# Kernel tuning notes

Measured on AMD Instinct MI355X. Metric: run time of the kernel, lower is better.

Reference implementation:

```python
import jax, jax.numpy as jnp
from jax import lax
import numpy as np

# TopoLoss(dim=1, p=2, topo_lambda=1.0)
# p=2 -> Euclidean ground metric for the Vietoris-Rips filtration.
# This reference computes the dominant H0 persistence diagram of the VR complex:
# for a point cloud, H0 births are all 0 and deaths are exactly the MST edge
# weights (Kruskal/union-find == Prim, computed here with a fixed-length scan).
# Wasserstein distance between the two diagrams (equal cardinality N-1, births 0)
# reduces to optimal 1D matching of the sorted death values (q=1, the
# torch_topological WassersteinDistance default).
TOPO_LAMBDA = 1.0
EPS = 1e-12


def _pairwise_euclidean(x):
    # x: [B, N, D] -> [B, N, N] via the Gram trick (avoids [B,N,N,D] temp)
    sq = jnp.sum(x * x, axis=-1)                      # [B, N]
    g = jnp.einsum('bnd,bmd->bnm', x, x)              # [B, N, N]
    d2 = sq[:, :, None] + sq[:, None, :] - 2.0 * g
    return jnp.sqrt(jnp.maximum(d2, 0.0) + EPS)


def _mst_deaths(D):
    # Prim's algorithm on a dense distance matrix D: [N, N].
    # Returns the sorted MST edge weights = H0 death times ([N-1]).
    N = D.shape[0]
    inf = jnp.asarray(jnp.inf, D.dtype)
    in_tree0 = jnp.zeros((N,), bool).at[0].set(True)
    min_dist0 = D[0]

    def step(carry, _):
        in_tree, min_dist = carry
        masked = jnp.where(in_tree, inf, min_dist)
        j = jnp.argmin(masked)
        death = masked[j]
        in_tree = in_tree.at[j].set(True)
        min_dist = jnp.minimum(min_dist, D[j])
        return (in_tree, min_dist), death

    _, deaths = lax.scan(step, (in_tree0, min_dist0), None, length=N - 1)
    return jnp.sort(deaths)


def _h0_diagram_deaths(x):
    # x: [B, N, D] -> sorted death values [B, N-1]
    D = _pairwise_euclidean(x)
    return jax.vmap(_mst_deaths)(D)


def setup_inputs() -> dict:
    key = jax.random.key(0)
    k1, k2 = jax.random.split(key)
    B, N, D = 64, 1024, 3
    gts = jax.random.normal(k1, (B, N, D), dtype=jnp.float32)
    preds = jax.random.normal(k2, (B, N, D), dtype=jnp.float32)
    return {"gts": gts, "preds": preds}


def reference(gts, preds):
    # note: source names pers_info_pred = complex(gts) (vars swapped there);
    # Wasserstein is symmetric so ordering is irrelevant.
    deaths_a = _h0_diagram_deaths(gts)    # [B, N-1]
    deaths_b = _h0_diagram_deaths(preds)  # [B, N-1]
    # W1 between diagrams with equal cardinality and births==0:
    # optimal matching of sorted death coordinates.
    per_batch = jnp.sum(jnp.abs(deaths_a - deaths_b), axis=-1)  # [B]
    return per_batch.mean() * TOPO_LAMBDA
```

## Files before the change

### kernel.cpp

```cpp
#include <hip/hip_runtime.h>
#include <math.h>

#define N 1024
#define T 1024
#define HALF 512
#define PHASE_CAP 10
#define SWITCH 80

typedef float v2f __attribute__((ext_vector_type(2)));
typedef unsigned long long ull;

#define INF64 0xFFFFFFFFFFFFFFFFull
#define INF32 0xFFFFFFFFu

__device__ __forceinline__ unsigned umin32(unsigned a, unsigned b) { return a < b ? a : b; }
__device__ __forceinline__ unsigned umax32(unsigned a, unsigned b) { return a > b ? a : b; }
__device__ __forceinline__ int imin32(int a, int b) { return a < b ? a : b; }

__device__ __forceinline__ unsigned walk_root(const unsigned* parent, unsigned x) {
    unsigned prev = x, cur = parent[x];
    while (cur != prev) {
        unsigned nxt = parent[cur];
        if (nxt == prev) { cur = umin32(cur, prev); break; }
        prev = cur; cur = nxt;
    }
    return cur;
}

#define DPP_MIN_SHR(v, sh)                                                                   \
    do {                                                                                     \
        unsigned _t = (unsigned)__builtin_amdgcn_update_dpp(                                 \
            (int)0xFFFFFFFF, (int)(v), 0x110 | (sh), 0xF, 0xF, false);                       \
        (v) = umin32((v), _t);                                                               \
    } while (0)

__global__ __launch_bounds__(T) void scan1_kernel(const float* __restrict__ gts,
                                                  const float* __restrict__ preds,
                                                  unsigned* __restrict__ bests1) {
    __shared__ float px[N], py[N], pz[N];
    __shared__ float stage[3 * N];
    __shared__ unsigned pb8[8][HALF];
    const int t = threadIdx.x;
    const int cloud = blockIdx.x >> 1;
    const int nh = blockIdx.x & 1;
    const float* __restrict__ src = (cloud < 64 ? gts : preds) + (size_t)(cloud & 63) * N * 3;

    if (t < 768) ((float4*)stage)[t] = ((const float4*)src)[t];
    __syncthreads();
    px[t] = stage[3 * t]; py[t] = stage[3 * t + 1]; pz[t] = stage[3 * t + 2];
    __syncthreads();

    const int q = t & 127;
    const int s = t >> 7;
    const int jbase = s << 7;
    const int n0 = nh * HALF + q;
    const int n1 = n0 + 128, n2 = n0 + 256, n3 = n0 + 384;
    const v2f axA = (v2f){px[n0], px[n1]}, ayA = (v2f){py[n0], py[n1]}, azA = (v2f){pz[n0], pz[n1]};
    const v2f axB = (v2f){px[n2], px[n3]}, ayB = (v2f){py[n2], py[n3]}, azB = (v2f){pz[n2], pz[n3]};
    unsigned b0 = INF32, b1 = INF32, b2 = INF32, b3 = INF32;
    #pragma unroll 4
    for (int jj = 0; jj < 128; jj += 2) {
        const int j = jbase + jj;
        v2f qx = *(const v2f*)&px[j];
        v2f qy = *(const v2f*)&py[j];
        v2f qz = *(const v2f*)&pz[j];
        #define STEP1(SX, SY, SZ, JV)                                                   \
        {                                                                               \
            const v2f sxv = (v2f){SX, SX}, syv = (v2f){SY, SY}, szv = (v2f){SZ, SZ};    \
            v2f dxA = axA - sxv, dyA = ayA - syv, dzA = azA - szv;                      \
            v2f eA = dxA * dxA;                                                         \
            eA = __builtin_elementwise_fma(dyA, dyA, eA);                               \
            eA = __builtin_elementwise_fma(dzA, dzA, eA);                               \
            v2f dxB = axB - sxv, dyB = ayB - syv, dzB = azB - szv;                      \
            v2f eB = dxB * dxB;                                                         \
            eB = __builtin_elementwise_fma(dyB, dyB, eB);                               \
            eB = __builtin_elementwise_fma(dzB, dzB, eB);                               \
            unsigned kk;                                                                \
            kk = (__float_as_uint(eA.x) & 0xFFFFF800u) | (unsigned)(JV);                \
            b0 = umin32(b0, ((JV) == n0) ? INF32 : kk);                                 \
            kk = (__float_as_uint(eA.y) & 0xFFFFF800u) | (unsigned)(JV);                \
            b1 = umin32(b1, ((JV) == n1) ? INF32 : kk);                                 \
            kk = (__float_as_uint(eB.x) & 0xFFFFF800u) | (unsigned)(JV);                \
            b2 = umin32(b2, ((JV) == n2) ? INF32 : kk);                                 \
            kk = (__float_as_uint(eB.y) & 0xFFFFF800u) | (unsigned)(JV);                \
            b3 = umin32(b3, ((JV) == n3) ? INF32 : kk);                                 \
        }
        STEP1(qx.x, qy.x, qz.x, j)
        STEP1(qx.y, qy.y, qz.y, j + 1)
        #undef STEP1
    }
    pb8[s][q] = b0; pb8[s][q + 128] = b1; pb8[s][q + 256] = b2; pb8[s][q + 384] = b3;
    __syncthreads();
    if (t < HALF) {
        unsigned best = umin32(umin32(pb8[0][t], pb8[1][t]), umin32(pb8[2][t], pb8[3][t]));
        best = umin32(best, umin32(umin32(pb8[4][t], pb8[5][t]), umin32(pb8[6][t], pb8[7][t])));
        bests1[(size_t)cloud * N + nh * HALF + t] = best;
    }
}

__global__ __launch_bounds__(T) void scan2_kernel(const float* __restrict__ gts,
                                                  const float* __restrict__ preds,
                                                  const unsigned* __restrict__ bests1,
                                                  unsigned* __restrict__ bests2) {
    __shared__ float px[N], py[N], pz[N];
    __shared__ float stage[3 * N];
    __shared__ unsigned cw[N];
    __shared__ unsigned parent[N];
    __shared__ unsigned pb8[8][HALF];
    const int t = threadIdx.x;
    const int cloud = blockIdx.x >> 1;
    const int nh = blockIdx.x & 1;
    const float* __restrict__ src = (cloud < 64 ? gts : preds) + (size_t)(cloud & 63) * N * 3;

    if (t < 768) ((float4*)stage)[t] = ((const float4*)src)[t];
    __syncthreads();
    px[t] = stage[3 * t]; py[t] = stage[3 * t + 1]; pz[t] = stage[3 * t + 2];
    parent[t] = bests1[(size_t)cloud * N + t] & 0x3FFu;
    __syncthreads();
    {
        unsigned r = walk_root(parent, (unsigned)t);
        parent[t] = r;
        cw[t] = r;
    }
    __syncthreads();

    const int q = t & 127;
    const int s = t >> 7;
    const int jbase = s << 7;
    const int n0 = nh * HALF + q;
    const int n1 = n0 + 128, n2 = n0 + 256, n3 = n0 + 384;
    const unsigned c0 = cw[n0], c1 = cw[n1], c2 = cw[n2], c3 = cw[n3];
    const v2f axA = (v2f){px[n0], px[n1]}, ayA = (v2f){py[n0], py[n1]}, azA = (v2f){pz[n0], pz[n1]};
    const v2f axB = (v2f){px[n2], px[n3]}, ayB = (v2f){py[n2], py[n3]}, azB = (v2f){pz[n2], pz[n3]};
    unsigned b0 = INF32, b1 = INF32, b2 = INF32, b3 = INF32;
    #pragma unroll 4
    for (int jj = 0; jj < 128; jj += 2) {
        const int j = jbase + jj;
        v2f qx = *(const v2f*)&px[j];
        v2f qy = *(const v2f*)&py[j];
        v2f qz = *(const v2f*)&pz[j];
        uint2 cj = *(const uint2*)&cw[j];
        #define STEP2(SX, SY, SZ, CJ, JV)                                               \
        {                                                                               \
            const v2f sxv = (v2f){SX, SX}, syv = (v2f){SY, SY}, szv = (v2f){SZ, SZ};    \
            v2f dxA = axA - sxv, dyA = ayA - syv, dzA = azA - szv;                      \
            v2f eA = dxA * dxA;                                                         \
            eA = __builtin_elementwise_fma(dyA, dyA, eA);                               \
            eA = __builtin_elementwise_fma(dzA, dzA, eA);                               \
            v2f dxB = axB - sxv, dyB = ayB - syv, dzB = azB - szv;                      \
            v2f eB = dxB * dxB;                                                         \
            eB = __builtin_elementwise_fma(dyB, dyB, eB);                               \
            eB = __builtin_elementwise_fma(dzB, dzB, eB);                               \
            unsigned kk;                                                                \
            kk = (__float_as_uint(eA.x) & 0xFFFFF800u) | (unsigned)(JV);                \
            b0 = umin32(b0, ((CJ) == c0) ? INF32 : kk);                                 \
            kk = (__float_as_uint(eA.y) & 0xFFFFF800u) | (unsigned)(JV);                \
            b1 = umin32(b1, ((CJ) == c1) ? INF32 : kk);                                 \
            kk = (__float_as_uint(eB.x) & 0xFFFFF800u) | (unsigned)(JV);                \
            b2 = umin32(b2, ((CJ) == c2) ? INF32 : kk);                                 \
            kk = (__float_as_uint(eB.y) & 0xFFFFF800u) | (unsigned)(JV);                \
            b3 = umin32(b3, ((CJ) == c3) ? INF32 : kk);                                 \
        }
        STEP2(qx.x, qy.x, qz.x, cj.x, j)
        STEP2(qx.y, qy.y, qz.y, cj.y, j + 1)
        #undef STEP2
    }
    pb8[s][q] = b0; pb8[s][q + 128] = b1; pb8[s][q + 256] = b2; pb8[s][q + 384] = b3;
    __syncthreads();
    if (t < HALF) {
        unsigned best = umin32(umin32(pb8[0][t], pb8[1][t]), umin32(pb8[2][t], pb8[3][t]));
        best = umin32(best, umin32(umin32(pb8[4][t], pb8[5][t]), umin32(pb8[6][t], pb8[7][t])));
        bests2[(size_t)cloud * N + nh * HALF + t] = best;
    }
}

__global__ __launch_bounds__(T) void final_kernel(const float* __restrict__ gts,
                                                  const float* __restrict__ preds,
                                                  float* __restrict__ ws,
                                                  const unsigned* __restrict__ bests1,
                                                  const unsigned* __restrict__ bests2,
                                                  int nPre) {
    __shared__ float4 pts[N];
    __shared__ float4 spts[N];
    __shared__ unsigned comp[N];
    __shared__ ull bestComp[N];
    __shared__ unsigned parent[N];
    __shared__ __align__(16) unsigned pb[2][N];
    __shared__ float deaths[N];
    __shared__ unsigned wsum[16];
    __shared__ int deathCount;

    const int t = threadIdx.x;
    const int blk = blockIdx.x;
    const float* __restrict__ src = (blk < 64 ? gts : preds) + (size_t)(blk & 63) * N * 3;

    {
        float* stg = (float*)&spts[0];
        if (t < 768) ((float4*)stg)[t] = ((const float4*)src)[t];
        __syncthreads();
        float x = stg[3 * t], y = stg[3 * t + 1], z = stg[3 * t + 2];
        pts[t] = make_float4(x, y, z, __uint_as_float((unsigned)t));
        comp[t] = (unsigned)t;
        parent[t] = (unsigned)t;
        deaths[t] = 0.0f;
        bestComp[t] = INF64;
    }
    if (t == 0) deathCount = 0;
    __syncthreads();

    const int n = t & (HALF - 1);
    const int h = t >> 9;
    const int n2 = n + HALF;
    const int jbase = h * HALF;
    float4 pA = pts[n], pB = pts[n2];
    const v2f pxv = (v2f){pA.x, pB.x};
    const v2f pyv = (v2f){pA.y, pB.y};
    const v2f pzv = (v2f){pA.z, pB.z};

    if (nPre >= 1) {
        unsigned b1 = bests1[(size_t)blk * N + t];
        unsigned j1 = b1 & 0x3FFu;
        unsigned e1 = b1 & 0xFFFFF800u;
        parent[t] = j1;
        __syncthreads();
        {
            unsigned p = j1;
            unsigned gp = parent[p];
            bool mutual = (gp == (unsigned)t);
            bool rec = !mutual || ((unsigned)t < p);
            float dval = rec ? sqrtf(__uint_as_float(e1) + 1e-12f) : 0.0f;
            ull m = __ballot(rec);
            int cnt = __popcll(m);
            int base = 0;
            if ((t & 63) == 0 && cnt) base = atomicAdd(&deathCount, cnt);
            base = __shfl(base, 0, 64);
            if (rec) {
                int idx = base + __popcll(m & ((1ull << (t & 63)) - 1ull));
                if (idx < N - 1) deaths[idx] = dval;
            }
        }
        __syncthreads();
        {
            unsigned r = walk_root(parent, (unsigned)t);
            parent[t] = r;
            comp[t] = r;
            pts[t].w = __uint_as_float(r);
        }
        __syncthreads();
    }

    if (nPre >= 2) {
        unsigned b2 = bests2[(size_t)blk * N + t];
        if (b2 != INF32) {
            unsigned j2 = b2 & 0x3FFu, e2 = b2 & 0xFFFFF800u;
            unsigned mn = umin32((unsigned)t, j2), mx = umax32((unsigned)t, j2);
            atomicMin(&bestComp[comp[t]], ((ull)e2 << 20) | (ull)((mn << 10) | mx));
        }
        __syncthreads();
        const unsigned c = (unsigned)t;
        const bool isRoot = (parent[c] == c);
        {
            ull bc = bestComp[c];
            if (isRoot && bc != INF64) {
                unsigned mn = (unsigned)((bc >> 10) & 0x3FFu);
                unsigned mx = (unsigned)(bc & 0x3FFu);
                unsigned cm = comp[mn];
                parent[c] = (cm == c) ? comp[mx] : cm;
            }
        }
        __syncthreads();
        {
            bool rec = false;
            float dval = 0.0f;
            unsigned p = parent[c];
            if (isRoot && p != c) {
                unsigned gp = parent[p];
                bool mutual = (gp == c);
                rec = !mutual || (c < p);
                if (rec) dval = sqrtf(__uint_as_float((unsigned)(bestComp[c] >> 20)) + 1e-12f);
            }
            ull m = __ballot(rec);
            int cnt = __popcll(m);
            int base = 0;
            if ((t & 63) == 0 && cnt) base = atomicAdd(&deathCount, cnt);
            base = __shfl(base, 0, 64);
            if (rec) {
                int idx = base + __popcll(m & ((1ull << (t & 63)) - 1ull));
                if (idx < N - 1) deaths[idx] = dval;
            }
        }
        __syncthreads();
        {
            unsigned r = walk_root(parent, c);
            parent[t] = r;
            unsigned nc = walk_root(parent, comp[t]);
            comp[t] = nc;
            pts[t].w = __uint_as_float(nc);
            bestComp[t] = INF64;
        }
        __syncthreads();
    }

    int phase = nPre;
    while (N - deathCount > SWITCH && phase < PHASE_CAP) {
        const unsigned c0 = comp[n], c1 = comp[n2];
        unsigned best0 = INF32, best1 = INF32;
        #pragma unroll 8
        for (int jj = 0; jj < HALF; ++jj) {
            int j = jbase + jj;
            float4 pj = pts[j];
            unsigned cj = __float_as_uint(pj.w);
            v2f dx = pxv - (v2f){pj.x, pj.x};
            v2f dy = pyv - (v2f){pj.y, pj.y};
            v2f dz = pzv - (v2f){pj.z, pj.z};
            v2f e = dx * dx;
            e = __builtin_elementwise_fma(dy, dy, e);
            e = __builtin_elementwise_fma(dz, dz, e);
            unsigned k0 = (__float_as_uint(e.x) & 0xFFFFF800u) | (unsigned)j;
            unsigned k1 = (__float_as_uint(e.y) & 0xFFFFF800u) | (unsigned)j;
            k0 = (cj == c0) ? INF32 : k0;
            k1 = (cj == c1) ? INF32 : k1;
            best0 = umin32(best0, k0);
            best1 = umin32(best1, k1);
        }
        pb[h][n] = best0;
        pb[h][n2] = best1;
        __syncthreads();
        if (h == 0) {
            #pragma unroll
            for (int s = 0; s < 2; ++s) {
                int m = s == 0 ? n : n2;
                unsigned fb = umin32(pb[0][m], pb[1][m]);
                if (fb != INF32) {
                    unsigned j = fb & 0x3FFu, e = fb & 0xFFFFF800u;
                    unsigned mn = umin32((unsigned)m, j), mx = umax32((unsigned)m, j);
                    ull key = ((ull)e << 20) | (ull)((mn << 10) | mx);
                    if (phase == 0) bestComp[m] = key;
                    else atomicMin(&bestComp[comp[m]], key);
                }
            }
        }
        __syncthreads();
        const unsigned c = (unsigned)t;
        const bool isRoot = (parent[c] == c);
        {
            ull bc = bestComp[c];
            if (isRoot && bc != INF64) {
                unsigned mn = (unsigned)((bc >> 10) & 0x3FFu);
                unsigned mx = (unsigned)(bc & 0x3FFu);
                unsigned cm = comp[mn];
                parent[c] = (cm == c) ? comp[mx] : cm;
            }
        }
        __syncthreads();
        {
            bool rec = false;
            float dval = 0.0f;
            unsigned p = parent[c];
            if (isRoot && p != c) {
                unsigned gp = parent[p];
                bool mutual = (gp == c);
                rec = !mutual || (c < p);
                if (rec) dval = sqrtf(__uint_as_float((unsigned)(bestComp[c] >> 20)) + 1e-12f);
            }
            ull m = __ballot(rec);
            int cnt = __popcll(m);
            int base = 0;
            if ((t & 63) == 0 && cnt) base = atomicAdd(&deathCount, cnt);
            base = __shfl(base, 0, 64);
            if (rec) {
                int idx = base + __popcll(m & ((1ull << (t & 63)) - 1ull));
                if (idx < N - 1) deaths[idx] = dval;
            }
        }
        __syncthreads();
        {
            unsigned r = walk_root(parent, c);
            parent[t] = r;
            unsigned nc = walk_root(parent, comp[t]);
            comp[t] = nc;
            pts[t].w = __uint_as_float(nc);
            bestComp[t] = INF64;
        }
        __syncthreads();
        ++phase;
    }

    const int dcbase = deathCount;
    const int comps = N - dcbase;
    if (comps > 1) {
        unsigned* scomp = &pb[0][0];
        unsigned* hist = &pb[1][0];
        unsigned* wavemin = &pb[1][0];
        uint2* segs = (uint2*)&bestComp[0];
        const int lane = t & 63;
        const int wid = t >> 6;

        hist[t] = 0;
        __syncthreads();
        atomicAdd(&hist[comp[t]], 1u);
        __syncthreads();
        unsigned cnt = hist[t];
        unsigned inc = cnt;
        #pragma unroll
        for (int d = 1; d < 64; d <<= 1) {
            unsigned u = __shfl_up(inc, d, 64);
            if (lane >= d) inc += u;
        }
        if (lane == 63) wsum[wid] = inc;
        __syncthreads();
        unsigned wof = 0;
        for (int i = 0; i < wid; ++i) wof += wsum[i];
        unsigned excl = wof + inc - cnt;
        if (cnt) { segs[t].x = excl; segs[t].y = excl + cnt; }
        __syncthreads();
        hist[t] = excl;
        __syncthreads();
        {
            unsigned pos = atomicAdd(&hist[comp[t]], 1u);
            spts[pos] = pts[t];
            scomp[pos] = comp[t];
        }
        __syncthreads();

        unsigned c_cur = comp[0];
        v2f pxv2 = (v2f){0.f, 0.f}, pyv2 = pxv2, pzv2 = pxv2;
        unsigned myc0 = 0, myc1 = 0, md0 = INF32, md1 = INF32;
        if (t < HALF) {
            float4 q0 = spts[t], q1 = spts[t + HALF];
            myc0 = scomp[t];
            myc1 = scomp[t + HALF];
            pxv2 = (v2f){q0.x, q1.x};
            pyv2 = (v2f){q0.y, q1.y};
            pzv2 = (v2f){q0.z, q1.z};
            if (myc0 == c_cur) pxv2.x = INFINITY;
            if (myc1 == c_cur) pxv2.y = INFINITY;
        }

        for (int step = 0; step < comps - 1; ++step) {
            if (t < HALF) {
                uint2 sg = segs[c_cur];
                const int jb = (int)sg.x, je = (int)sg.y, jl = je - 1;
                for (int base = jb; base < je; base += 4) {
                    float4 q0 = spts[base];
                    float4 q1 = spts[imin32(base + 1, jl)];
                    float4 q2 = spts[imin32(base + 2, jl)];
                    float4 q3 = spts[imin32(base + 3, jl)];
                    #define RELAX(qq)                                                        \
                        {                                                                    \
                            v2f dx = pxv2 - (v2f){qq.x, qq.x};                               \
                            v2f dy = pyv2 - (v2f){qq.y, qq.y};                               \
                            v2f dz = pzv2 - (v2f){qq.z, qq.z};                               \
                            v2f e = dx * dx;                                                 \
                            e = __builtin_elementwise_fma(dy, dy, e);                        \
                            e = __builtin_elementwise_fma(dz, dz, e);                        \
                            md0 = umin32(md0, (__float_as_uint(e.x) & 0xFFFFFC00u) | myc0);  \
                            md1 = umin32(md1, (__float_as_uint(e.y) & 0xFFFFFC00u) | myc1);  \
                        }
                    RELAX(q0) RELAX(q1) RELAX(q2) RELAX(q3)
                    #undef RELAX
                }
                unsigned v = umin32(md0, md1);
                DPP_MIN_SHR(v, 1);
                DPP_MIN_SHR(v, 2);
                DPP_MIN_SHR(v, 4);
                DPP_MIN_SHR(v, 8);
                unsigned r0 = (unsigned)__builtin_amdgcn_readlane((int)v, 15);
                unsigned r1 = (unsigned)__builtin_amdgcn_readlane((int)v, 31);
                unsigned r2 = (unsigned)__builtin_amdgcn_readlane((int)v, 47);
                unsigned r3 = (unsigned)__builtin_amdgcn_readlane((int)v, 63);
                if (lane == 0)
                    wavemin[(step & 1) * 8 + wid] = umin32(umin32(r0, r1), umin32(r2, r3));
            }
            __syncthreads();
            if (t < HALF) {
                const uint4* wmv = (const uint4*)(wavemin + (step & 1) * 8);
                uint4 u0 = wmv[0], u1 = wmv[1];
                unsigned m0 = umin32(umin32(u0.x, u0.y), umin32(u0.z, u0.w));
                unsigned m1 = umin32(umin32(u1.x, u1.y), umin32(u1.z, u1.w));
                unsigned G = umin32(m0, m1);
                c_cur = G & 0x3FFu;
                if (t == 0)
                    deaths[dcbase + step] = sqrtf(__uint_as_float(G & 0xFFFFFC00u) + 1e-12f);
                if (myc0 == c_cur) { pxv2.x = INFINITY; md0 = INF32; }
                if (myc1 == c_cur) { pxv2.y = INFINITY; md1 = INF32; }
            }
        }
    }

    if (t == 0) deaths[N - 1] = INFINITY;
    __syncthreads();
    {
        float v = deaths[t];
        #pragma unroll
        for (int k = 2; k <= N; k <<= 1) {
            const bool up = ((t & k) == 0);
            #pragma unroll
            for (int j = k >> 1; j > 0; j >>= 1) {
                float u;
                if (j >= 64) {
                    deaths[t] = v;
                    __syncthreads();
                    u = deaths[t ^ j];
                    __syncthreads();
                } else {
                    u = __shfl_xor(v, j, 64);
                }
                v = (((t & j) == 0) == up) ? fminf(v, u) : fmaxf(v, u);
            }
        }
        float* dst = ws + (size_t)blk * N;
        dst[t] = (t < N - 1) ? v : 0.0f;
    }
}

__global__ __launch_bounds__(256) void diff_kernel(const float* __restrict__ ws,
                                                   float* __restrict__ out) {
    __shared__ float red[4];
    const int t = threadIdx.x;
    const int b = blockIdx.x;
    const float* a = ws + (size_t)b * N;
    const float* c = ws + (size_t)(64 + b) * N;
    float sum = 0.0f;
    for (int i = t; i < N; i += 256)
        sum += fabsf(a[i] - c[i]);
    #pragma unroll
    for (int off = 32; off > 0; off >>= 1)
        sum += __shfl_down(sum, off, 64);
    if ((t & 63) == 0) red[t >> 6] = sum;
    __syncthreads();
    if (t == 0)
        atomicAdd(out, (red[0] + red[1] + red[2] + red[3]) * (1.0f / 64.0f));
}

extern "C" void kernel_launch(void* const* d_in, const int* in_sizes, int n_in,
                              void* d_out, int out_size, void* d_ws, size_t ws_size,
                              hipStream_t stream) {
    const float* gts = (const float*)d_in[0];
    const float* preds = (const float*)d_in[1];
    float* ws = (float*)d_ws;
    unsigned* bests1 = (unsigned*)d_ws;
    unsigned* bests2 = bests1 + 128 * N;
    const bool big = ws_size >= (size_t)(2u * 128u * N * 4u);

    if (big) {
        hipLaunchKernelGGL(scan1_kernel, dim3(256), dim3(T), 0, stream, gts, preds, bests1);
        hipLaunchKernelGGL(scan2_kernel, dim3(256), dim3(T), 0, stream, gts, preds, bests1, bests2);
        hipLaunchKernelGGL(final_kernel, dim3(128), dim3(T), 0, stream,
                           gts, preds, ws, bests1, bests2, 2);
    } else {
        hipLaunchKernelGGL(final_kernel, dim3(128), dim3(T), 0, stream,
                           gts, preds, ws, (const unsigned*)nullptr, (const unsigned*)nullptr, 0);
    }
    hipMemsetAsync(d_out, 0, sizeof(float), stream);
    hipLaunchKernelGGL(diff_kernel, dim3(64), dim3(256), 0, stream, ws, (float*)d_out);
}
```

Baseline: 219.4 us.

## Fuse scan1, scan2 and final kernels into one cooperative kernel with grid syncs

Merges the three per-cloud kernels into a single cooperative launch of 256 blocks, using grid-wide syncs between stages and a union of the shared-memory layouts. The aim is to cut two kernel launch gaps and the pipeline drain between stages. In exchange, the final stage runs on only 128 of the 256 resident blocks, and grid sync adds its own cost. If the cooperative launch fails, the code falls back to the old three-kernel path.

```diff
diff --git a/kernel.cpp b/kernel.cpp
--- a/kernel.cpp
+++ b/kernel.cpp
@@ -1,4 +1,5 @@
 #include <hip/hip_runtime.h>
+#include <hip/hip_cooperative_groups.h>
 #include <math.h>
 
 #define N 1024
@@ -34,20 +35,35 @@
         (v) = umin32((v), _t);                                                               \
     } while (0)
 
-__global__ __launch_bounds__(T) void scan1_kernel(const float* __restrict__ gts,
-                                                  const float* __restrict__ preds,
-                                                  unsigned* __restrict__ bests1) {
-    __shared__ float px[N], py[N], pz[N];
-    __shared__ float stage[3 * N];
-    __shared__ unsigned pb8[8][HALF];
-    const int t = threadIdx.x;
-    const int cloud = blockIdx.x >> 1;
-    const int nh = blockIdx.x & 1;
-    const float* __restrict__ src = (cloud < 64 ? gts : preds) + (size_t)(cloud & 63) * N * 3;
-
-    if (t < 768) ((float4*)stage)[t] = ((const float4*)src)[t];
-    __syncthreads();
-    px[t] = stage[3 * t]; py[t] = stage[3 * t + 1]; pz[t] = stage[3 * t + 2];
+struct ScanShared {
+    float px[N], py[N], pz[N];
+    float stage[3 * N];
+    unsigned cw[N];
+    unsigned parent[N];
+    unsigned pb8[8][HALF];
+};
+struct FinalShared {
+    float4 pts[N];
+    float4 spts[N];
+    unsigned comp[N];
+    ull bestComp[N];
+    unsigned parent[N];
+    unsigned pb[2][N];
+    float deaths[N];
+    unsigned wsum[16];
+    int deathCount;
+};
+union MegaShared {
+    ScanShared s;
+    FinalShared f;
+};
+
+__device__ __forceinline__ void scan1_body(ScanShared& S, const float* __restrict__ src,
+                                           unsigned* __restrict__ bests1,
+                                           int cloud, int nh, int t) {
+    if (t < 768) ((float4*)S.stage)[t] = ((const float4*)src)[t];
+    __syncthreads();
+    S.px[t] = S.stage[3 * t]; S.py[t] = S.stage[3 * t + 1]; S.pz[t] = S.stage[3 * t + 2];
     __syncthreads();
 
     const int q = t & 127;
@@ -55,15 +71,17 @@
     const int jbase = s << 7;
     const int n0 = nh * HALF + q;
     const int n1 = n0 + 128, n2 = n0 + 256, n3 = n0 + 384;
-    const v2f axA = (v2f){px[n0], px[n1]}, ayA = (v2f){py[n0], py[n1]}, azA = (v2f){pz[n0], pz[n1]};
-    const v2f axB = (v2f){px[n2], px[n3]}, ayB = (v2f){py[n2], py[n3]}, azB = (v2f){pz[n2], pz[n3]};
+    const v2f axA = (v2f){S.px[n0], S.px[n1]}, ayA = (v2f){S.py[n0], S.py[n1]},
+              azA = (v2f){S.pz[n0], S.pz[n1]};
+    const v2f axB = (v2f){S.px[n2], S.px[n3]}, ayB = (v2f){S.py[n2], S.py[n3]},
+              azB = (v2f){S.pz[n2], S.pz[n3]};
     unsigned b0 = INF32, b1 = INF32, b2 = INF32, b3 = INF32;
     #pragma unroll 4
     for (int jj = 0; jj < 128; jj += 2) {
         const int j = jbase + jj;
-        v2f qx = *(const v2f*)&px[j];
-        v2f qy = *(const v2f*)&py[j];
-        v2f qz = *(const v2f*)&pz[j];
+        v2f qx = *(const v2f*)&S.px[j];
+        v2f qy = *(const v2f*)&S.py[j];
+        v2f qz = *(const v2f*)&S.pz[j];
         #define STEP1(SX, SY, SZ, JV)                                                   \
         {                                                                               \
             const v2f sxv = (v2f){SX, SX}, syv = (v2f){SY, SY}, szv = (v2f){SZ, SZ};    \
@@ -89,38 +107,29 @@
         STEP1(qx.y, qy.y, qz.y, j + 1)
         #undef STEP1
     }
-    pb8[s][q] = b0; pb8[s][q + 128] = b1; pb8[s][q + 256] = b2; pb8[s][q + 384] = b3;
+    S.pb8[s][q] = b0; S.pb8[s][q + 128] = b1; S.pb8[s][q + 256] = b2; S.pb8[s][q + 384] = b3;
     __syncthreads();
     if (t < HALF) {
-        unsigned best = umin32(umin32(pb8[0][t], pb8[1][t]), umin32(pb8[2][t], pb8[3][t]));
-        best = umin32(best, umin32(umin32(pb8[4][t], pb8[5][t]), umin32(pb8[6][t], pb8[7][t])));
+        unsigned best = umin32(umin32(S.pb8[0][t], S.pb8[1][t]), umin32(S.pb8[2][t], S.pb8[3][t]));
+        best = umin32(best, umin32(umin32(S.pb8[4][t], S.pb8[5][t]),
+                                   umin32(S.pb8[6][t], S.pb8[7][t])));
         bests1[(size_t)cloud * N + nh * HALF + t] = best;
     }
 }
 
-__global__ __launch_bounds__(T) void scan2_kernel(const float* __restrict__ gts,
-                                                  const float* __restrict__ preds,
-                                                  const unsigned* __restrict__ bests1,
-                                                  unsigned* __restrict__ bests2) {
-    __shared__ float px[N], py[N], pz[N];
-    __shared__ float stage[3 * N];
-    __shared__ unsigned cw[N];
-    __shared__ unsigned parent[N];
-    __shared__ unsigned pb8[8][HALF];
-    const int t = threadIdx.x;
-    const int cloud = blockIdx.x >> 1;
-    const int nh = blockIdx.x & 1;
-    const float* __restrict__ src = (cloud < 64 ? gts : preds) + (size_t)(cloud & 63) * N * 3;
-
-    if (t < 768) ((float4*)stage)[t] = ((const float4*)src)[t];
-    __syncthreads();
-    px[t] = stage[3 * t]; py[t] = stage[3 * t + 1]; pz[t] = stage[3 * t + 2];
-    parent[t] = bests1[(size_t)cloud * N + t] & 0x3FFu;
+__device__ __forceinline__ void scan2_body(ScanShared& S, const float* __restrict__ src,
+                                           const unsigned* __restrict__ bests1,
+                                           unsigned* __restrict__ bests2,
+                                           int cloud, int nh, int t) {
+    if (t < 768) ((float4*)S.stage)[t] = ((const float4*)src)[t];
+    __syncthreads();
+    S.px[t] = S.stage[3 * t]; S.py[t] = S.stage[3 * t + 1]; S.pz[t] = S.stage[3 * t + 2];
+    S.parent[t] = bests1[(size_t)cloud * N + t] & 0x3FFu;
     __syncthreads();
     {
-        unsigned r = walk_root(parent, (unsigned)t);
-        parent[t] = r;
-        cw[t] = r;
+        unsigned r = walk_root(S.parent, (unsigned)t);
+        S.parent[t] = r;
+        S.cw[t] = r;
     }
     __syncthreads();
 
@@ -129,17 +138,19 @@
     const int jbase = s << 7;
     const int n0 = nh * HALF + q;
     const int n1 = n0 + 128, n2 = n0 + 256, n3 = n0 + 384;
-    const unsigned c0 = cw[n0], c1 = cw[n1], c2 = cw[n2], c3 = cw[n3];
-    const v2f axA = (v2f){px[n0], px[n1]}, ayA = (v2f){py[n0], py[n1]}, azA = (v2f){pz[n0], pz[n1]};
-    const v2f axB = (v2f){px[n2], px[n3]}, ayB = (v2f){py[n2], py[n3]}, azB = (v2f){pz[n2], pz[n3]};
+    const unsigned c0 = S.cw[n0], c1 = S.cw[n1], c2 = S.cw[n2], c3 = S.cw[n3];
+    const v2f axA = (v2f){S.px[n0], S.px[n1]}, ayA = (v2f){S.py[n0], S.py[n1]},
+              azA = (v2f){S.pz[n0], S.pz[n1]};
+    const v2f axB = (v2f){S.px[n2], S.px[n3]}, ayB = (v2f){S.py[n2], S.py[n3]},
+              azB = (v2f){S.pz[n2], S.pz[n3]};
     unsigned b0 = INF32, b1 = INF32, b2 = INF32, b3 = INF32;
     #pragma unroll 4
     for (int jj = 0; jj < 128; jj += 2) {
         const int j = jbase + jj;
-        v2f qx = *(const v2f*)&px[j];
-        v2f qy = *(const v2f*)&py[j];
-        v2f qz = *(const v2f*)&pz[j];
-        uint2 cj = *(const uint2*)&cw[j];
+        v2f qx = *(const v2f*)&S.px[j];
+        v2f qy = *(const v2f*)&S.py[j];
+        v2f qz = *(const v2f*)&S.pz[j];
+        uint2 cj = *(const uint2*)&S.cw[j];
         #define STEP2(SX, SY, SZ, CJ, JV)                                               \
         {                                                                               \
             const v2f sxv = (v2f){SX, SX}, syv = (v2f){SY, SY}, szv = (v2f){SZ, SZ};    \
@@ -165,54 +176,40 @@
         STEP2(qx.y, qy.y, qz.y, cj.y, j + 1)
         #undef STEP2
     }
-    pb8[s][q] = b0; pb8[s][q + 128] = b1; pb8[s][q + 256] = b2; pb8[s][q + 384] = b3;
+    S.pb8[s][q] = b0; S.pb8[s][q + 128] = b1; S.pb8[s][q + 256] = b2; S.pb8[s][q + 384] = b3;
     __syncthreads();
     if (t < HALF) {
-        unsigned best = umin32(umin32(pb8[0][t], pb8[1][t]), umin32(pb8[2][t], pb8[3][t]));
-        best = umin32(best, umin32(umin32(pb8[4][t], pb8[5][t]), umin32(pb8[6][t], pb8[7][t])));
+        unsigned best = umin32(umin32(S.pb8[0][t], S.pb8[1][t]), umin32(S.pb8[2][t], S.pb8[3][t]));
+        best = umin32(best, umin32(umin32(S.pb8[4][t], S.pb8[5][t]),
+                                   umin32(S.pb8[6][t], S.pb8[7][t])));
         bests2[(size_t)cloud * N + nh * HALF + t] = best;
     }
 }
 
-__global__ __launch_bounds__(T) void final_kernel(const float* __restrict__ gts,
-                                                  const float* __restrict__ preds,
-                                                  float* __restrict__ ws,
-                                                  const unsigned* __restrict__ bests1,
-                                                  const unsigned* __restrict__ bests2,
-                                                  int nPre) {
-    __shared__ float4 pts[N];
-    __shared__ float4 spts[N];
-    __shared__ unsigned comp[N];
-    __shared__ ull bestComp[N];
-    __shared__ unsigned parent[N];
-    __shared__ __align__(16) unsigned pb[2][N];
-    __shared__ float deaths[N];
-    __shared__ unsigned wsum[16];
-    __shared__ int deathCount;
-
-    const int t = threadIdx.x;
-    const int blk = blockIdx.x;
-    const float* __restrict__ src = (blk < 64 ? gts : preds) + (size_t)(blk & 63) * N * 3;
-
+__device__ void final_body(FinalShared& S, const float* __restrict__ src,
+                           float* __restrict__ ws,
+                           const unsigned* __restrict__ bests1,
+                           const unsigned* __restrict__ bests2,
+                           int nPre, int blk, int t) {
     {
-        float* stg = (float*)&spts[0];
+        float* stg = (float*)&S.spts[0];
         if (t < 768) ((float4*)stg)[t] = ((const float4*)src)[t];
         __syncthreads();
         float x = stg[3 * t], y = stg[3 * t + 1], z = stg[3 * t + 2];
-        pts[t] = make_float4(x, y, z, __uint_as_float((unsigned)t));
-        comp[t] = (unsigned)t;
-        parent[t] = (unsigned)t;
-        deaths[t] = 0.0f;
-        bestComp[t] = INF64;
-    }
-    if (t == 0) deathCount = 0;
+        S.pts[t] = make_float4(x, y, z, __uint_as_float((unsigned)t));
+        S.comp[t] = (unsigned)t;
+        S.parent[t] = (unsigned)t;
+        S.deaths[t] = 0.0f;
+        S.bestComp[t] = INF64;
+    }
+    if (t == 0) S.deathCount = 0;
     __syncthreads();
 
     const int n = t & (HALF - 1);
     const int h = t >> 9;
     const int n2 = n + HALF;
     const int jbase = h * HALF;
-    float4 pA = pts[n], pB = pts[n2];
+    float4 pA = S.pts[n], pB = S.pts[n2];
     const v2f pxv = (v2f){pA.x, pB.x};
     const v2f pyv = (v2f){pA.y, pB.y};
     const v2f pzv = (v2f){pA.z, pB.z};
@@ -221,30 +218,30 @@
         unsigned b1 = bests1[(size_t)blk * N + t];
         unsigned j1 = b1 & 0x3FFu;
         unsigned e1 = b1 & 0xFFFFF800u;
-        parent[t] = j1;
+        S.parent[t] = j1;
         __syncthreads();
         {
             unsigned p = j1;
-            unsigned gp = parent[p];
+            unsigned gp = S.parent[p];
             bool mutual = (gp == (unsigned)t);
             bool rec = !mutual || ((unsigned)t < p);
             float dval = rec ? sqrtf(__uint_as_float(e1) + 1e-12f) : 0.0f;
             ull m = __ballot(rec);
             int cnt = __popcll(m);
             int base = 0;
-            if ((t & 63) == 0 && cnt) base = atomicAdd(&deathCount, cnt);
+            if ((t & 63) == 0 && cnt) base = atomicAdd(&S.deathCount, cnt);
             base = __shfl(base, 0, 64);
             if (rec) {
                 int idx = base + __popcll(m & ((1ull << (t & 63)) - 1ull));
-                if (idx < N - 1) deaths[idx] = dval;
-            }
-        }
-        __syncthreads();
-        {
-            unsigned r = walk_root(parent, (unsigned)t);
-            parent[t] = r;
-            comp[t] = r;
-            pts[t].w = __uint_as_float(r);
+                if (idx < N - 1) S.deaths[idx] = dval;
+            }
+        }
+        __syncthreads();
+        {
+            unsigned r = walk_root(S.parent, (unsigned)t);
+            S.parent[t] = r;
+            S.comp[t] = r;
+            S.pts[t].w = __uint_as_float(r);
         }
         __syncthreads();
     }
@@ -254,61 +251,61 @@
         if (b2 != INF32) {
             unsigned j2 = b2 & 0x3FFu, e2 = b2 & 0xFFFFF800u;
             unsigned mn = umin32((unsigned)t, j2), mx = umax32((unsigned)t, j2);
-            atomicMin(&bestComp[comp[t]], ((ull)e2 << 20) | (ull)((mn << 10) | mx));
+            atomicMin(&S.bestComp[S.comp[t]], ((ull)e2 << 20) | (ull)((mn << 10) | mx));
         }
         __syncthreads();
         const unsigned c = (unsigned)t;
-        const bool isRoot = (parent[c] == c);
-        {
-            ull bc = bestComp[c];
+        const bool isRoot = (S.parent[c] == c);
+        {
+            ull bc = S.bestComp[c];
             if (isRoot && bc != INF64) {
                 unsigned mn = (unsigned)((bc >> 10) & 0x3FFu);
                 unsigned mx = (unsigned)(bc & 0x3FFu);
-                unsigned cm = comp[mn];
-                parent[c] = (cm == c) ? comp[mx] : cm;
+                unsigned cm = S.comp[mn];
+                S.parent[c] = (cm == c) ? S.comp[mx] : cm;
             }
         }
         __syncthreads();
         {
             bool rec = false;
             float dval = 0.0f;
-            unsigned p = parent[c];
+            unsigned p = S.parent[c];
             if (isRoot && p != c) {
-                unsigned gp = parent[p];
+                unsigned gp = S.parent[p];
                 bool mutual = (gp == c);
                 rec = !mutual || (c < p);
-                if (rec) dval = sqrtf(__uint_as_float((unsigned)(bestComp[c] >> 20)) + 1e-12f);
+                if (rec) dval = sqrtf(__uint_as_float((unsigned)(S.bestComp[c] >> 20)) + 1e-12f);
             }
             ull m = __ballot(rec);
             int cnt = __popcll(m);
             int base = 0;
-            if ((t & 63) == 0 && cnt) base = atomicAdd(&deathCount, cnt);
+            if ((t & 63) == 0 && cnt) base = atomicAdd(&S.deathCount, cnt);
             base = __shfl(base, 0, 64);
             if (rec) {
                 int idx = base + __popcll(m & ((1ull << (t & 63)) - 1ull));
-                if (idx < N - 1) deaths[idx] = dval;
-            }
-        }
-        __syncthreads();
-        {
-            unsigned r = walk_root(parent, c);
-            parent[t] = r;
-            unsigned nc = walk_root(parent, comp[t]);
-            comp[t] = nc;
-            pts[t].w = __uint_as_float(nc);
-            bestComp[t] = INF64;
+                if (idx < N - 1) S.deaths[idx] = dval;
+            }
+        }
+        __syncthreads();
+        {
+            unsigned r = walk_root(S.parent, c);
+            S.parent[t] = r;
+            unsigned nc = walk_root(S.parent, S.comp[t]);
+            S.comp[t] = nc;
+            S.pts[t].w = __uint_as_float(nc);
+            S.bestComp[t] = INF64;
         }
         __syncthreads();
     }
 
     int phase = nPre;
-    while (N - deathCount > SWITCH && phase < PHASE_CAP) {
-        const unsigned c0 = comp[n], c1 = comp[n2];
+    while (N - S.deathCount > SWITCH && phase < PHASE_CAP) {
+        const unsigned c0 = S.comp[n], c1 = S.comp[n2];
         unsigned best0 = INF32, best1 = INF32;
         #pragma unroll 8
         for (int jj = 0; jj < HALF; ++jj) {
             int j = jbase + jj;
-            float4 pj = pts[j];
+            float4 pj = S.pts[j];
             unsigned cj = __float_as_uint(pj.w);
             v2f dx = pxv - (v2f){pj.x, pj.x};
             v2f dy = pyv - (v2f){pj.y, pj.y};
@@ -323,82 +320,82 @@
             best0 = umin32(best0, k0);
             best1 = umin32(best1, k1);
         }
-        pb[h][n] = best0;
-        pb[h][n2] = best1;
+        S.pb[h][n] = best0;
+        S.pb[h][n2] = best1;
         __syncthreads();
         if (h == 0) {
             #pragma unroll
             for (int s = 0; s < 2; ++s) {
                 int m = s == 0 ? n : n2;
-                unsigned fb = umin32(pb[0][m], pb[1][m]);
+                unsigned fb = umin32(S.pb[0][m], S.pb[1][m]);
                 if (fb != INF32) {
                     unsigned j = fb & 0x3FFu, e = fb & 0xFFFFF800u;
                     unsigned mn = umin32((unsigned)m, j), mx = umax32((unsigned)m, j);
                     ull key = ((ull)e << 20) | (ull)((mn << 10) | mx);
-                    if (phase == 0) bestComp[m] = key;
-                    else atomicMin(&bestComp[comp[m]], key);
+                    if (phase == 0) S.bestComp[m] = key;
+                    else atomicMin(&S.bestComp[S.comp[m]], key);
                 }
             }
         }
         __syncthreads();
         const unsigned c = (unsigned)t;
-        const bool isRoot = (parent[c] == c);
-        {
-            ull bc = bestComp[c];
+        const bool isRoot = (S.parent[c] == c);
+        {
+            ull bc = S.bestComp[c];
             if (isRoot && bc != INF64) {
                 unsigned mn = (unsigned)((bc >> 10) & 0x3FFu);
                 unsigned mx = (unsigned)(bc & 0x3FFu);
-                unsigned cm = comp[mn];
-                parent[c] = (cm == c) ? comp[mx] : cm;
+                unsigned cm = S.comp[mn];
+                S.parent[c] = (cm == c) ? S.comp[mx] : cm;
             }
         }
         __syncthreads();
         {
             bool rec = false;
             float dval = 0.0f;
-            unsigned p = parent[c];
+            unsigned p = S.parent[c];
             if (isRoot && p != c) {
-                unsigned gp = parent[p];
+                unsigned gp = S.parent[p];
                 bool mutual = (gp == c);
                 rec = !mutual || (c < p);
-                if (rec) dval = sqrtf(__uint_as_float((unsigned)(bestComp[c] >> 20)) + 1e-12f);
+                if (rec) dval = sqrtf(__uint_as_float((unsigned)(S.bestComp[c] >> 20)) + 1e-12f);
             }
             ull m = __ballot(rec);
             int cnt = __popcll(m);
             int base = 0;
-            if ((t & 63) == 0 && cnt) base = atomicAdd(&deathCount, cnt);
+            if ((t & 63) == 0 && cnt) base = atomicAdd(&S.deathCount, cnt);
             base = __shfl(base, 0, 64);
             if (rec) {
                 int idx = base + __popcll(m & ((1ull << (t & 63)) - 1ull));
-                if (idx < N - 1) deaths[idx] = dval;
-            }
-        }
-        __syncthreads();
-        {
-            unsigned r = walk_root(parent, c);
-            parent[t] = r;
-            unsigned nc = walk_root(parent, comp[t]);
-            comp[t] = nc;
-            pts[t].w = __uint_as_float(nc);
-            bestComp[t] = INF64;
+                if (idx < N - 1) S.deaths[idx] = dval;
+            }
+        }
+        __syncthreads();
+        {
+            unsigned r = walk_root(S.parent, c);
+            S.parent[t] = r;
+            unsigned nc = walk_root(S.parent, S.comp[t]);
+            S.comp[t] = nc;
+            S.pts[t].w = __uint_as_float(nc);
+            S.bestComp[t] = INF64;
         }
         __syncthreads();
         ++phase;
     }
 
-    const int dcbase = deathCount;
+    const int dcbase = S.deathCount;
     const int comps = N - dcbase;
     if (comps > 1) {
-        unsigned* scomp = &pb[0][0];
-        unsigned* hist = &pb[1][0];
-        unsigned* wavemin = &pb[1][0];
-        uint2* segs = (uint2*)&bestComp[0];
+        unsigned* scomp = &S.pb[0][0];
+        unsigned* hist = &S.pb[1][0];
+        unsigned* wavemin = &S.pb[1][0];
+        uint2* segs = (uint2*)&S.bestComp[0];
         const int lane = t & 63;
         const int wid = t >> 6;
 
         hist[t] = 0;
         __syncthreads();
-        atomicAdd(&hist[comp[t]], 1u);
+        atomicAdd(&hist[S.comp[t]], 1u);
         __syncthreads();
         unsigned cnt = hist[t];
         unsigned inc = cnt;
@@ -407,27 +404,27 @@
             unsigned u = __shfl_up(inc, d, 64);
             if (lane >= d) inc += u;
         }
-        if (lane == 63) wsum[wid] = inc;
+        if (lane == 63) S.wsum[wid] = inc;
         __syncthreads();
         unsigned wof = 0;
-        for (int i = 0; i < wid; ++i) wof += wsum[i];
+        for (int i = 0; i < wid; ++i) wof += S.wsum[i];
         unsigned excl = wof + inc - cnt;
         if (cnt) { segs[t].x = excl; segs[t].y = excl + cnt; }
         __syncthreads();
         hist[t] = excl;
         __syncthreads();
         {
-            unsigned pos = atomicAdd(&hist[comp[t]], 1u);
-            spts[pos] = pts[t];
-            scomp[pos] = comp[t];
-        }
-        __syncthreads();
-
-        unsigned c_cur = comp[0];
+            unsigned pos = atomicAdd(&hist[S.comp[t]], 1u);
+            S.spts[pos] = S.pts[t];
+            scomp[pos] = S.comp[t];
+        }
+        __syncthreads();
+
+        unsigned c_cur = S.comp[0];
         v2f pxv2 = (v2f){0.f, 0.f}, pyv2 = pxv2, pzv2 = pxv2;
         unsigned myc0 = 0, myc1 = 0, md0 = INF32, md1 = INF32;
         if (t < HALF) {
-            float4 q0 = spts[t], q1 = spts[t + HALF];
+            float4 q0 = S.spts[t], q1 = S.spts[t + HALF];
             myc0 = scomp[t];
             myc1 = scomp[t + HALF];
             pxv2 = (v2f){q0.x, q1.x};
@@ -442,10 +439,10 @@
                 uint2 sg = segs[c_cur];
                 const int jb = (int)sg.x, je = (int)sg.y, jl = je - 1;
                 for (int base = jb; base < je; base += 4) {
-                    float4 q0 = spts[base];
-                    float4 q1 = spts[imin32(base + 1, jl)];
-                    float4 q2 = spts[imin32(base + 2, jl)];
-                    float4 q3 = spts[imin32(base + 3, jl)];
+                    float4 q0 = S.spts[base];
+                    float4 q1 = S.spts[imin32(base + 1, jl)];
+                    float4 q2 = S.spts[imin32(base + 2, jl)];
+                    float4 q3 = S.spts[imin32(base + 3, jl)];
                     #define RELAX(qq)                                                        \
                         {                                                                    \
                             v2f dx = pxv2 - (v2f){qq.x, qq.x};                               \
@@ -481,17 +478,17 @@
                 unsigned G = umin32(m0, m1);
                 c_cur = G & 0x3FFu;
                 if (t == 0)
-                    deaths[dcbase + step] = sqrtf(__uint_as_float(G & 0xFFFFFC00u) + 1e-12f);
+                    S.deaths[dcbase + step] = sqrtf(__uint_as_float(G & 0xFFFFFC00u) + 1e-12f);
                 if (myc0 == c_cur) { pxv2.x = INFINITY; md0 = INF32; }
                 if (myc1 == c_cur) { pxv2.y = INFINITY; md1 = INF32; }
             }
         }
     }
 
-    if (t == 0) deaths[N - 1] = INFINITY;
+    if (t == 0) S.deaths[N - 1] = INFINITY;
     __syncthreads();
     {
-        float v = deaths[t];
+        float v = S.deaths[t];
         #pragma unroll
         for (int k = 2; k <= N; k <<= 1) {
             const bool up = ((t & k) == 0);
@@ -499,9 +496,9 @@
             for (int j = k >> 1; j > 0; j >>= 1) {
                 float u;
                 if (j >= 64) {
-                    deaths[t] = v;
+                    S.deaths[t] = v;
                     __syncthreads();
-                    u = deaths[t ^ j];
+                    u = S.deaths[t ^ j];
                     __syncthreads();
                 } else {
                     u = __shfl_xor(v, j, 64);
@@ -512,6 +509,65 @@
         float* dst = ws + (size_t)blk * N;
         dst[t] = (t < N - 1) ? v : 0.0f;
     }
+}
+
+__global__ __launch_bounds__(T) void mega_kernel(const float* __restrict__ gts,
+                                                 const float* __restrict__ preds,
+                                                 float* __restrict__ ws,
+                                                 unsigned* __restrict__ bests1,
+                                                 unsigned* __restrict__ bests2) {
+    __shared__ MegaShared u;
+    const int t = threadIdx.x;
+    const int b = blockIdx.x;
+
+    {
+        const int cloud = b >> 1, nh = b & 1;
+        const float* src = (cloud < 64 ? gts : preds) + (size_t)(cloud & 63) * N * 3;
+        scan1_body(u.s, src, bests1, cloud, nh, t);
+    }
+    __threadfence();
+    cooperative_groups::this_grid().sync();
+    __threadfence();
+    {
+        const int cloud = b >> 1, nh = b & 1;
+        const float* src = (cloud < 64 ? gts : preds) + (size_t)(cloud & 63) * N * 3;
+        scan2_body(u.s, src, bests1, bests2, cloud, nh, t);
+    }
+    __threadfence();
+    cooperative_groups::this_grid().sync();
+    __threadfence();
+    if (b >= 128) return;
+    const float* src = (b < 64 ? gts : preds) + (size_t)(b & 63) * N * 3;
+    final_body(u.f, src, ws, bests1, bests2, 2, b, t);
+}
+
+__global__ __launch_bounds__(T) void scan1_kernel(const float* __restrict__ gts,
+                                                  const float* __restrict__ preds,
+                                                  unsigned* __restrict__ bests1) {
+    __shared__ ScanShared S;
+    const int cloud = blockIdx.x >> 1, nh = blockIdx.x & 1;
+    const float* src = (cloud < 64 ? gts : preds) + (size_t)(cloud & 63) * N * 3;
+    scan1_body(S, src, bests1, cloud, nh, threadIdx.x);
+}
+__global__ __launch_bounds__(T) void scan2_kernel(const float* __restrict__ gts,
+                                                  const float* __restrict__ preds,
+                                                  const unsigned* __restrict__ bests1,
+                                                  unsigned* __restrict__ bests2) {
+    __shared__ ScanShared S;
+    const int cloud = blockIdx.x >> 1, nh = blockIdx.x & 1;
+    const float* src = (cloud < 64 ? gts : preds) + (size_t)(cloud & 63) * N * 3;
+    scan2_body(S, src, bests1, bests2, cloud, nh, threadIdx.x);
+}
+__global__ __launch_bounds__(T) void final_kernel(const float* __restrict__ gts,
+                                                  const float* __restrict__ preds,
+                                                  float* __restrict__ ws,
+                                                  const unsigned* __restrict__ bests1,
+                                                  const unsigned* __restrict__ bests2,
+                                                  int nPre) {
+    __shared__ FinalShared S;
+    const int blk = blockIdx.x;
+    const float* src = (blk < 64 ? gts : preds) + (size_t)(blk & 63) * N * 3;
+    final_body(S, src, ws, bests1, bests2, nPre, blk, threadIdx.x);
 }
 
 __global__ __launch_bounds__(256) void diff_kernel(const float* __restrict__ ws,
@@ -544,10 +600,21 @@
     const bool big = ws_size >= (size_t)(2u * 128u * N * 4u);
 
     if (big) {
-        hipLaunchKernelGGL(scan1_kernel, dim3(256), dim3(T), 0, stream, gts, preds, bests1);
-        hipLaunchKernelGGL(scan2_kernel, dim3(256), dim3(T), 0, stream, gts, preds, bests1, bests2);
-        hipLaunchKernelGGL(final_kernel, dim3(128), dim3(T), 0, stream,
-                           gts, preds, ws, bests1, bests2, 2);
+        void* args[5];
+        args[0] = (void*)&gts;
+        args[1] = (void*)&preds;
+        args[2] = (void*)&ws;
+        args[3] = (void*)&bests1;
+        args[4] = (void*)&bests2;
+        hipError_t cerr = hipLaunchCooperativeKernel((const void*)mega_kernel,
+                                                     dim3(256), dim3(T), args, 0, stream);
+        if (cerr != hipSuccess) {
+            hipLaunchKernelGGL(scan1_kernel, dim3(256), dim3(T), 0, stream, gts, preds, bests1);
+            hipLaunchKernelGGL(scan2_kernel, dim3(256), dim3(T), 0, stream,
+                               gts, preds, bests1, bests2);
+            hipLaunchKernelGGL(final_kernel, dim3(128), dim3(T), 0, stream,
+                               gts, preds, ws, bests1, bests2, 2);
+        }
     } else {
         hipLaunchKernelGGL(final_kernel, dim3(128), dim3(T), 0, stream,
                            gts, preds, ws, (const unsigned*)nullptr, (const unsigned*)nullptr, 0);
```

New measurement: 518.9 us. +136.5%, slower.

## Split scan kernels into quarter blocks and fuse final diff reduction into last block

Applied to the files above, without the earlier changes.

Each scan kernel block now handles 256 query points, two per thread, instead of 512, four per thread, and the grid doubles to 512 blocks so work spreads across more CUs. The separate diff kernel launch is replaced by a last-block-done tail in final_kernel: blocks take a ticket via an atomic on the output word, and the last block computes the Wasserstein sum and overwrites the output. The output memset moves before the launches. The Boruvka loop threshold also changes when no prescans ran. The trade-off is redundant point loading per block, plus reliance on a ticket counter stored in the output buffer.

```diff
diff --git a/kernel.cpp b/kernel.cpp
--- a/kernel.cpp
+++ b/kernel.cpp
@@ -39,10 +39,10 @@
                                                   unsigned* __restrict__ bests1) {
     __shared__ float px[N], py[N], pz[N];
     __shared__ float stage[3 * N];
-    __shared__ unsigned pb8[8][HALF];
+    __shared__ unsigned pb8[8][256];
     const int t = threadIdx.x;
-    const int cloud = blockIdx.x >> 1;
-    const int nh = blockIdx.x & 1;
+    const int cloud = blockIdx.x >> 2;
+    const int qr = blockIdx.x & 3;
     const float* __restrict__ src = (cloud < 64 ? gts : preds) + (size_t)(cloud & 63) * N * 3;
 
     if (t < 768) ((float4*)stage)[t] = ((const float4*)src)[t];
@@ -53,11 +53,11 @@
     const int q = t & 127;
     const int s = t >> 7;
     const int jbase = s << 7;
-    const int n0 = nh * HALF + q;
-    const int n1 = n0 + 128, n2 = n0 + 256, n3 = n0 + 384;
-    const v2f axA = (v2f){px[n0], px[n1]}, ayA = (v2f){py[n0], py[n1]}, azA = (v2f){pz[n0], pz[n1]};
-    const v2f axB = (v2f){px[n2], px[n3]}, ayB = (v2f){py[n2], py[n3]}, azB = (v2f){pz[n2], pz[n3]};
-    unsigned b0 = INF32, b1 = INF32, b2 = INF32, b3 = INF32;
+    const int n0 = qr * 256 + q;
+    const int n1 = n0 + 128;
+    const v2f axv = (v2f){px[n0], px[n1]}, ayv = (v2f){py[n0], py[n1]},
+              azv = (v2f){pz[n0], pz[n1]};
+    unsigned b0 = INF32, b1 = INF32;
     #pragma unroll 4
     for (int jj = 0; jj < 128; jj += 2) {
         const int j = jbase + jj;
@@ -67,34 +67,26 @@
         #define STEP1(SX, SY, SZ, JV)                                                   \
         {                                                                               \
             const v2f sxv = (v2f){SX, SX}, syv = (v2f){SY, SY}, szv = (v2f){SZ, SZ};    \
-            v2f dxA = axA - sxv, dyA = ayA - syv, dzA = azA - szv;                      \
-            v2f eA = dxA * dxA;                                                         \
-            eA = __builtin_elementwise_fma(dyA, dyA, eA);                               \
-            eA = __builtin_elementwise_fma(dzA, dzA, eA);                               \
-            v2f dxB = axB - sxv, dyB = ayB - syv, dzB = azB - szv;                      \
-            v2f eB = dxB * dxB;                                                         \
-            eB = __builtin_elementwise_fma(dyB, dyB, eB);                               \
-            eB = __builtin_elementwise_fma(dzB, dzB, eB);                               \
-            unsigned kk;                                                                \
-            kk = (__float_as_uint(eA.x) & 0xFFFFF800u) | (unsigned)(JV);                \
-            b0 = umin32(b0, ((JV) == n0) ? INF32 : kk);                                 \
-            kk = (__float_as_uint(eA.y) & 0xFFFFF800u) | (unsigned)(JV);                \
-            b1 = umin32(b1, ((JV) == n1) ? INF32 : kk);                                 \
-            kk = (__float_as_uint(eB.x) & 0xFFFFF800u) | (unsigned)(JV);                \
-            b2 = umin32(b2, ((JV) == n2) ? INF32 : kk);                                 \
-            kk = (__float_as_uint(eB.y) & 0xFFFFF800u) | (unsigned)(JV);                \
-            b3 = umin32(b3, ((JV) == n3) ? INF32 : kk);                                 \
+            v2f dx = axv - sxv, dy = ayv - syv, dz = azv - szv;                         \
+            v2f e = dx * dx;                                                            \
+            e = __builtin_elementwise_fma(dy, dy, e);                                   \
+            e = __builtin_elementwise_fma(dz, dz, e);                                   \
+            unsigned k0 = (__float_as_uint(e.x) & 0xFFFFF800u) | (unsigned)(JV);        \
+            unsigned k1 = (__float_as_uint(e.y) & 0xFFFFF800u) | (unsigned)(JV);        \
+            b0 = umin32(b0, ((JV) == n0) ? INF32 : k0);                                 \
+            b1 = umin32(b1, ((JV) == n1) ? INF32 : k1);                                 \
         }
         STEP1(qx.x, qy.x, qz.x, j)
         STEP1(qx.y, qy.y, qz.y, j + 1)
         #undef STEP1
     }
-    pb8[s][q] = b0; pb8[s][q + 128] = b1; pb8[s][q + 256] = b2; pb8[s][q + 384] = b3;
-    __syncthreads();
-    if (t < HALF) {
+    pb8[s][q] = b0;
+    pb8[s][q + 128] = b1;
+    __syncthreads();
+    if (t < 256) {
         unsigned best = umin32(umin32(pb8[0][t], pb8[1][t]), umin32(pb8[2][t], pb8[3][t]));
         best = umin32(best, umin32(umin32(pb8[4][t], pb8[5][t]), umin32(pb8[6][t], pb8[7][t])));
-        bests1[(size_t)cloud * N + nh * HALF + t] = best;
+        bests1[(size_t)cloud * N + qr * 256 + t] = best;
     }
 }
 
@@ -106,10 +98,10 @@
     __shared__ float stage[3 * N];
     __shared__ unsigned cw[N];
     __shared__ unsigned parent[N];
-    __shared__ unsigned pb8[8][HALF];
+    __shared__ unsigned pb8[8][256];
     const int t = threadIdx.x;
-    const int cloud = blockIdx.x >> 1;
-    const int nh = blockIdx.x & 1;
+    const int cloud = blockIdx.x >> 2;
+    const int qr = blockIdx.x & 3;
     const float* __restrict__ src = (cloud < 64 ? gts : preds) + (size_t)(cloud & 63) * N * 3;
 
     if (t < 768) ((float4*)stage)[t] = ((const float4*)src)[t];
@@ -127,12 +119,12 @@
     const int q = t & 127;
     const int s = t >> 7;
     const int jbase = s << 7;
-    const int n0 = nh * HALF + q;
-    const int n1 = n0 + 128, n2 = n0 + 256, n3 = n0 + 384;
-    const unsigned c0 = cw[n0], c1 = cw[n1], c2 = cw[n2], c3 = cw[n3];
-    const v2f axA = (v2f){px[n0], px[n1]}, ayA = (v2f){py[n0], py[n1]}, azA = (v2f){pz[n0], pz[n1]};
-    const v2f axB = (v2f){px[n2], px[n3]}, ayB = (v2f){py[n2], py[n3]}, azB = (v2f){pz[n2], pz[n3]};
-    unsigned b0 = INF32, b1 = INF32, b2 = INF32, b3 = INF32;
+    const int n0 = qr * 256 + q;
+    const int n1 = n0 + 128;
+    const unsigned c0 = cw[n0], c1 = cw[n1];
+    const v2f axv = (v2f){px[n0], px[n1]}, ayv = (v2f){py[n0], py[n1]},
+              azv = (v2f){pz[n0], pz[n1]};
+    unsigned b0 = INF32, b1 = INF32;
     #pragma unroll 4
     for (int jj = 0; jj < 128; jj += 2) {
         const int j = jbase + jj;
@@ -143,34 +135,26 @@
         #define STEP2(SX, SY, SZ, CJ, JV)                                               \
         {                                                                               \
             const v2f sxv = (v2f){SX, SX}, syv = (v2f){SY, SY}, szv = (v2f){SZ, SZ};    \
-            v2f dxA = axA - sxv, dyA = ayA - syv, dzA = azA - szv;                      \
-            v2f eA = dxA * dxA;                                                         \
-            eA = __builtin_elementwise_fma(dyA, dyA, eA);                               \
-            eA = __builtin_elementwise_fma(dzA, dzA, eA);                               \
-            v2f dxB = axB - sxv, dyB = ayB - syv, dzB = azB - szv;                      \
-            v2f eB = dxB * dxB;                                                         \
-            eB = __builtin_elementwise_fma(dyB, dyB, eB);                               \
-            eB = __builtin_elementwise_fma(dzB, dzB, eB);                               \
-            unsigned kk;                                                                \
-            kk = (__float_as_uint(eA.x) & 0xFFFFF800u) | (unsigned)(JV);                \
-            b0 = umin32(b0, ((CJ) == c0) ? INF32 : kk);                                 \
-            kk = (__float_as_uint(eA.y) & 0xFFFFF800u) | (unsigned)(JV);                \
-            b1 = umin32(b1, ((CJ) == c1) ? INF32 : kk);                                 \
-            kk = (__float_as_uint(eB.x) & 0xFFFFF800u) | (unsigned)(JV);                \
-            b2 = umin32(b2, ((CJ) == c2) ? INF32 : kk);                                 \
-            kk = (__float_as_uint(eB.y) & 0xFFFFF800u) | (unsigned)(JV);                \
-            b3 = umin32(b3, ((CJ) == c3) ? INF32 : kk);                                 \
+            v2f dx = axv - sxv, dy = ayv - syv, dz = azv - szv;                         \
+            v2f e = dx * dx;                                                            \
+            e = __builtin_elementwise_fma(dy, dy, e);                                   \
+            e = __builtin_elementwise_fma(dz, dz, e);                                   \
+            unsigned k0 = (__float_as_uint(e.x) & 0xFFFFF800u) | (unsigned)(JV);        \
+            unsigned k1 = (__float_as_uint(e.y) & 0xFFFFF800u) | (unsigned)(JV);        \
+            b0 = umin32(b0, ((CJ) == c0) ? INF32 : k0);                                 \
+            b1 = umin32(b1, ((CJ) == c1) ? INF32 : k1);                                 \
         }
         STEP2(qx.x, qy.x, qz.x, cj.x, j)
         STEP2(qx.y, qy.y, qz.y, cj.y, j + 1)
         #undef STEP2
     }
-    pb8[s][q] = b0; pb8[s][q + 128] = b1; pb8[s][q + 256] = b2; pb8[s][q + 384] = b3;
-    __syncthreads();
-    if (t < HALF) {
+    pb8[s][q] = b0;
+    pb8[s][q + 128] = b1;
+    __syncthreads();
+    if (t < 256) {
         unsigned best = umin32(umin32(pb8[0][t], pb8[1][t]), umin32(pb8[2][t], pb8[3][t]));
         best = umin32(best, umin32(umin32(pb8[4][t], pb8[5][t]), umin32(pb8[6][t], pb8[7][t])));
-        bests2[(size_t)cloud * N + nh * HALF + t] = best;
+        bests2[(size_t)cloud * N + qr * 256 + t] = best;
     }
 }
 
@@ -179,7 +163,9 @@
                                                   float* __restrict__ ws,
                                                   const unsigned* __restrict__ bests1,
                                                   const unsigned* __restrict__ bests2,
-                                                  int nPre) {
+                                                  int nPre,
+                                                  float* __restrict__ out,
+                                                  int doTail) {
     __shared__ float4 pts[N];
     __shared__ float4 spts[N];
     __shared__ unsigned comp[N];
@@ -189,6 +175,8 @@
     __shared__ float deaths[N];
     __shared__ unsigned wsum[16];
     __shared__ int deathCount;
+    __shared__ int ticketS;
+    __shared__ float redT[2][4][4];
 
     const int t = threadIdx.x;
     const int blk = blockIdx.x;
@@ -302,7 +290,7 @@
     }
 
     int phase = nPre;
-    while (N - deathCount > SWITCH && phase < PHASE_CAP) {
+    while (N - deathCount > (nPre ? SWITCH : 1) && phase < PHASE_CAP) {
         const unsigned c0 = comp[n], c1 = comp[n2];
         unsigned best0 = INF32, best1 = INF32;
         #pragma unroll 8
@@ -512,6 +500,39 @@
         float* dst = ws + (size_t)blk * N;
         dst[t] = (t < N - 1) ? v : 0.0f;
     }
+
+    if (doTail) {
+        __threadfence();
+        __syncthreads();
+        if (t == 0) ticketS = (int)atomicAdd((unsigned*)out, 1u);
+        __syncthreads();
+        if (ticketS == 127) {
+            __threadfence();
+            const int g = t >> 8, tl = t & 255;
+            float acc = 0.0f;
+            for (int chunk = 0; chunk < 16; ++chunk) {
+                const int b = (chunk << 2) + g;
+                const float* a = ws + (size_t)b * N;
+                const float* c = ws + (size_t)(64 + b) * N;
+                float sum = 0.0f;
+                for (int i = tl; i < N; i += 256)
+                    sum += fabsf(a[i] - c[i]);
+                #pragma unroll
+                for (int off = 32; off > 0; off >>= 1)
+                    sum += __shfl_down(sum, off, 64);
+                if ((tl & 63) == 0) redT[chunk & 1][g][tl >> 6] = sum;
+                __syncthreads();
+                if (t == 0) {
+                    #pragma unroll
+                    for (int gg = 0; gg < 4; ++gg) {
+                        const float* r = redT[chunk & 1][gg];
+                        acc += (r[0] + r[1] + r[2] + r[3]) * (1.0f / 64.0f);
+                    }
+                }
+            }
+            if (t == 0) out[0] = acc;
+        }
+    }
 }
 
 __global__ __launch_bounds__(256) void diff_kernel(const float* __restrict__ ws,
@@ -543,15 +564,16 @@
     unsigned* bests2 = bests1 + 128 * N;
     const bool big = ws_size >= (size_t)(2u * 128u * N * 4u);
 
+    hipMemsetAsync(d_out, 0, sizeof(float), stream);
     if (big) {
-        hipLaunchKernelGGL(scan1_kernel, dim3(256), dim3(T), 0, stream, gts, preds, bests1);
-        hipLaunchKernelGGL(scan2_kernel, dim3(256), dim3(T), 0, stream, gts, preds, bests1, bests2);
+        hipLaunchKernelGGL(scan1_kernel, dim3(512), dim3(T), 0, stream, gts, preds, bests1);
+        hipLaunchKernelGGL(scan2_kernel, dim3(512), dim3(T), 0, stream, gts, preds, bests1, bests2);
         hipLaunchKernelGGL(final_kernel, dim3(128), dim3(T), 0, stream,
-                           gts, preds, ws, bests1, bests2, 2);
+                           gts, preds, ws, bests1, bests2, 2, (float*)d_out, 1);
     } else {
         hipLaunchKernelGGL(final_kernel, dim3(128), dim3(T), 0, stream,
-                           gts, preds, ws, (const unsigned*)nullptr, (const unsigned*)nullptr, 0);
-    }
-    hipMemsetAsync(d_out, 0, sizeof(float), stream);
-    hipLaunchKernelGGL(diff_kernel, dim3(64), dim3(256), 0, stream, ws, (float*)d_out);
+                           gts, preds, ws, (const unsigned*)nullptr, (const unsigned*)nullptr, 0,
+                           (float*)d_out, 0);
+        hipLaunchKernelGGL(diff_kernel, dim3(64), dim3(256), 0, stream, ws, (float*)d_out);
+    }
 }
```

Measured after the change: 272.5 us. 1.24x slower.
